# Optimization experiments

Measured on AMD Instinct MI355X. Metric: run time of the kernel, lower is better.

The kernel has to match this reference:

```python
import jax, jax.numpy as jnp
import numpy as np

HIDDEN = 512
HEADS = 8
PREFIX = 1  # prefix_size: rows >= PREFIX may not attend to cols < PREFIX (except causal tril already zeroed those only partially)


def setup_inputs() -> dict:
    key = jax.random.key(0)
    k1, k2, k3 = jax.random.split(key, 3)
    B, L, D = 2, 4096, HIDDEN
    x = jax.random.normal(k1, (B, L, D), dtype=jnp.float32)
    # torch Linear(hidden, 3*hidden): y = x @ W^T + b; we store W^T directly as [D, 3D]
    w_in = jax.random.normal(k2, (D, 3 * D), dtype=jnp.float32) * (1.0 / np.sqrt(D))
    b_in = jnp.zeros((3 * D,), dtype=jnp.float32)
    w_out = jax.random.normal(k3, (D, D), dtype=jnp.float32) * (1.0 / np.sqrt(D))
    b_out = jnp.zeros((D,), dtype=jnp.float32)
    return {"x": x, "w_in": w_in, "b_in": b_in, "w_out": w_out, "b_out": b_out}


def _prefix_causal_mask(L):
    # tril(ones) then zero out [prefix:, :prefix]
    m = jnp.tril(jnp.ones((L, L), dtype=bool))
    m = m.at[PREFIX:, :PREFIX].set(False)
    return m  # True = attend allowed


def reference(x, w_in, b_in, w_out, b_out):
    B, L, D = x.shape
    H, hd = HEADS, D // HEADS
    qkv = x @ w_in + b_in  # [B, L, 3D]
    q, k, v = jnp.split(qkv, 3, axis=-1)
    q = q.reshape(B, L, H, hd).transpose(0, 2, 1, 3)  # [B,H,L,hd]
    k = k.reshape(B, L, H, hd).transpose(0, 2, 1, 3)
    v = v.reshape(B, L, H, hd).transpose(0, 2, 1, 3)
    scale = 1.0 / np.sqrt(hd).astype(np.float32)
    attn = jnp.einsum('bhqd,bhkd->bhqk', q, k) * scale  # [B,H,L,L]
    mask = _prefix_causal_mask(L)
    attn = jnp.where(mask[None, None, :, :], attn, -jnp.inf)
    attn = jax.nn.softmax(attn, axis=-1)  # dropout p=0.0 -> identity
    out = jnp.einsum('bhqk,bhkd->bhqd', attn, v)  # [B,H,L,hd]
    out = out.transpose(0, 2, 1, 3).reshape(B, L, D)
    return out @ w_out + b_out
```

## Files before the change

kernel.cpp:

```cpp
#include <hip/hip_runtime.h>
#include <hip/hip_bf16.h>

#define BSZ   2
#define LSEQ  4096
#define DH    512
#define NH    8
#define HDIM  64

typedef unsigned short ushort_t;
typedef __attribute__((ext_vector_type(8))) short s8v;
typedef __attribute__((ext_vector_type(4))) short s4v;
typedef __attribute__((ext_vector_type(4))) float f4v;

#define C_EXP 0.18033688011112042f

__device__ __forceinline__ ushort_t f2bf(float f) {
    __hip_bfloat16 h = __float2bfloat16(f);
    return *(ushort_t*)&h;
}

__device__ __forceinline__ unsigned int fbits(float f) {
    union { float f; unsigned int u; } c; c.f = f; return c.u;
}

__device__ __forceinline__ unsigned int pk_trunc(float lo, float hi) {
    return (fbits(lo) >> 16) | (fbits(hi) & 0xFFFF0000u);
}

__device__ __forceinline__ void gld_lds16(const ushort_t* g, ushort_t* l) {
    __builtin_amdgcn_global_load_lds(
        (const __attribute__((address_space(1))) void*)g,
        (__attribute__((address_space(3))) void*)l, 16, 0, 0);
}

__device__ __forceinline__ void transpose_tile(const float* __restrict__ src,
                                               ushort_t* __restrict__ dst,
                                               int R, int C, int bx, int by)
{
    __shared__ float tile[32][33];
    int r0 = by * 32, c0 = bx * 32;
    int t = threadIdx.x;
    int tr = t >> 5, tc = t & 31;
    #pragma unroll
    for (int i = 0; i < 4; i++)
        tile[tr + 8 * i][tc] = src[(size_t)(r0 + tr + 8 * i) * C + c0 + tc];
    __syncthreads();
    #pragma unroll
    for (int i = 0; i < 4; i++) {
        int oc = tr + 8 * i;
        dst[(size_t)(c0 + oc) * R + r0 + tc] = f2bf(tile[tc][oc]);
    }
}

__global__ __launch_bounds__(256) void prep(const float* __restrict__ x,
                                            ushort_t* __restrict__ xb,
                                            const float* __restrict__ w_in,
                                            ushort_t* __restrict__ w_inT,
                                            const float* __restrict__ w_out,
                                            ushort_t* __restrict__ w_outT,
                                            float* __restrict__ Oacc,
                                            float* __restrict__ lacc)
{
    int bx = blockIdx.x;
    if (bx < 4096) {
        int i = (bx * 256 + threadIdx.x) * 4;
        float4 v = *(const float4*)&x[i];
        ushort_t o[4] = {f2bf(v.x), f2bf(v.y), f2bf(v.z), f2bf(v.w)};
        *(uint2*)&xb[i] = *(uint2*)o;
    } else if (bx < 4864) {
        int idx = bx - 4096;
        transpose_tile(w_in, w_inT, DH, 3 * DH, idx % 48, idx / 48);
    } else if (bx < 5120) {
        int idx = bx - 4864;
        transpose_tile(w_out, w_outT, DH, DH, idx % 16, idx / 16);
    } else if (bx < 9216) {
        int i = ((bx - 5120) * 256 + threadIdx.x) * 4;
        float4 z = {0.f, 0.f, 0.f, 0.f};
        *(float4*)&Oacc[i] = z;
    } else {
        int i = ((bx - 9216) * 256 + threadIdx.x) * 4;
        float4 z = {0.f, 0.f, 0.f, 0.f};
        *(float4*)&lacc[i] = z;
    }
}

template <typename OUT, bool QSCALE, bool VTRANS>
__global__ __launch_bounds__(256) void gemm_bt(const ushort_t* __restrict__ A,
                                               const ushort_t* __restrict__ Bt,
                                               const float* __restrict__ bias,
                                               OUT* __restrict__ C,
                                               ushort_t* __restrict__ vtout,
                                               int M, int N, int K)
{
    __shared__ ushort_t As[128 * 32];
    __shared__ ushort_t Bs[128 * 32];
    const int tid = threadIdx.x;
    const int row0 = blockIdx.y * 128, col0 = blockIdx.x * 128;
    const int wid = tid >> 6, lane = tid & 63;
    const int wm = wid >> 1, wn = wid & 1;
    const int quad = lane >> 4, ln = lane & 15;

    f4v acc[4][4] = {};

    const int srow = (lane >> 2);
    const int scol = (lane & 3) * 8;

    for (int k0 = 0; k0 < K; k0 += 32) {
        #pragma unroll
        for (int t = 0; t < 2; t++) {
            int chunk = wid * 2 + t;
            int r = chunk * 16 + srow;
            gld_lds16(&A[(size_t)(row0 + r) * K + k0 + scol], &As[chunk * 512]);
            gld_lds16(&Bt[(size_t)(col0 + r) * K + k0 + scol], &Bs[chunk * 512]);
        }
        __syncthreads();
        s8v af[4], bf[4];
        #pragma unroll
        for (int mt = 0; mt < 4; mt++)
            af[mt] = *(const s8v*)&As[(wm * 64 + mt * 16 + ln) * 32 + quad * 8];
        #pragma unroll
        for (int nt = 0; nt < 4; nt++)
            bf[nt] = *(const s8v*)&Bs[(wn * 64 + nt * 16 + ln) * 32 + quad * 8];
        #pragma unroll
        for (int mt = 0; mt < 4; mt++)
            #pragma unroll
            for (int nt = 0; nt < 4; nt++)
                acc[mt][nt] = __builtin_amdgcn_mfma_f32_16x16x32_bf16(
                    af[mt], bf[nt], acc[mt][nt], 0, 0, 0);
        __syncthreads();
    }

    #pragma unroll
    for (int mt = 0; mt < 4; mt++) {
        #pragma unroll
        for (int nt = 0; nt < 4; nt++) {
            int c = col0 + wn * 64 + nt * 16 + ln;
            float bv = bias[c];
            float scl = 1.0f;
            if constexpr (QSCALE) scl = (c < DH) ? C_EXP : 1.0f;
            bool vcol = false;
            if constexpr (VTRANS) vcol = (c >= 2 * DH);
            if (vcol) {
                int d = c - 2 * DH;
                int hh = d >> 6, dd = d & 63;
                int r0 = row0 + wm * 64 + mt * 16 + quad * 4;
                int bb = r0 >> 12, l = r0 & (LSEQ - 1);
                ushort_t tmp[4];
                #pragma unroll
                for (int reg = 0; reg < 4; reg++)
                    tmp[reg] = f2bf(acc[mt][nt][reg] + bv);
                *(uint2*)&vtout[((size_t)((bb * NH + hh) * 64 + dd)) * LSEQ + l]
                    = *(uint2*)tmp;
            } else {
                #pragma unroll
                for (int reg = 0; reg < 4; reg++) {
                    int r = row0 + wm * 64 + mt * 16 + quad * 4 + reg;
                    float v = (acc[mt][nt][reg] + bv) * scl;
                    if constexpr (sizeof(OUT) == 2)
                        C[(size_t)r * N + c] = (OUT)f2bf(v);
                    else
                        C[(size_t)r * N + c] = v;
                }
            }
        }
    }
}

__global__ __launch_bounds__(128) void flash_mfma(const ushort_t* __restrict__ qkv,
                                                  const ushort_t* __restrict__ vt,
                                                  float* __restrict__ Oacc,
                                                  float* __restrict__ lacc)
{
    __shared__ ushort_t Ks[64 * 72];
    __shared__ ushort_t Vs[64 * 72];

    const int p     = blockIdx.x >> 1;
    const int khalf = blockIdx.x & 1;
    const int h = blockIdx.y, b = blockIdx.z;
    const int tid = threadIdx.x;
    const int w = tid >> 6, lane = tid & 63;
    const int quad = lane >> 4, ln = lane & 15;

    const int sr = tid >> 1, sc = (tid & 1) * 32;
    const int ldsw = sr * 72 + sc;
    const size_t kstep = (size_t)64 * 3 * DH;

    const int qts[2] = {63 - p, p};

    for (int ti = 0; ti < 2; ti++) {
        const int qt = qts[ti], q0 = qt * 64;
        const int qrow0 = q0 + w * 32;
        const int n = qt + 1;
        const int ktBeg = khalf ? ((n + 1) >> 1) : 0;
        const int ktEnd = khalf ? n : ((n + 1) >> 1);

        s8v qa[2][2];
        #pragma unroll
        for (int qg = 0; qg < 2; qg++) {
            const ushort_t* qrow = qkv
                + ((size_t)(b * LSEQ + qrow0 + qg * 16 + ln)) * (3 * DH) + h * HDIM;
            qa[qg][0] = *(const s8v*)(qrow + quad * 8);
            qa[qg][1] = *(const s8v*)(qrow + 32 + quad * 8);
        }

        float l_s[2] = {0.0f, 0.0f};
        f4v o_acc[2][4] = {};

        if (ktBeg < ktEnd) {
            size_t gk = ((size_t)(b * LSEQ + ktBeg * 64 + sr)) * (3 * DH) + DH + h * HDIM + sc;
            size_t gv = ((size_t)((b * NH + h) * 64 + sr)) * LSEQ + ktBeg * 64 + sc;
            uint4 pk0 = *(const uint4*)&qkv[gk];
            uint4 pk1 = *(const uint4*)&qkv[gk + 8];
            uint4 pk2 = *(const uint4*)&qkv[gk + 16];
            uint4 pk3 = *(const uint4*)&qkv[gk + 24];
            uint4 pv0 = *(const uint4*)&vt[gv];
            uint4 pv1 = *(const uint4*)&vt[gv + 8];
            uint4 pv2 = *(const uint4*)&vt[gv + 16];
            uint4 pv3 = *(const uint4*)&vt[gv + 24];

            for (int kt = ktBeg; kt < ktEnd; kt++) {
                const int k0 = kt * 64;
                __syncthreads();
                *(uint4*)&Ks[ldsw]      = pk0;
                *(uint4*)&Ks[ldsw + 8]  = pk1;
                *(uint4*)&Ks[ldsw + 16] = pk2;
                *(uint4*)&Ks[ldsw + 24] = pk3;
                *(uint4*)&Vs[ldsw]      = pv0;
                *(uint4*)&Vs[ldsw + 8]  = pv1;
                *(uint4*)&Vs[ldsw + 16] = pv2;
                *(uint4*)&Vs[ldsw + 24] = pv3;
                if (kt + 1 < ktEnd) {
                    gk += kstep; gv += 64;
                    pk0 = *(const uint4*)&qkv[gk];
                    pk1 = *(const uint4*)&qkv[gk + 8];
                    pk2 = *(const uint4*)&qkv[gk + 16];
                    pk3 = *(const uint4*)&qkv[gk + 24];
                    pv0 = *(const uint4*)&vt[gv];
                    pv1 = *(const uint4*)&vt[gv + 8];
                    pv2 = *(const uint4*)&vt[gv + 16];
                    pv3 = *(const uint4*)&vt[gv + 24];
                }
                __syncthreads();

                s8v kb[4][2];
                #pragma unroll
                for (int nt = 0; nt < 4; nt++) {
                    kb[nt][0] = *(const s8v*)&Ks[(nt * 16 + ln) * 72 + quad * 8];
                    kb[nt][1] = *(const s8v*)&Ks[(nt * 16 + ln) * 72 + 32 + quad * 8];
                }
                s4v vf[4][4];
                #pragma unroll
                for (int dt = 0; dt < 4; dt++)
                    #pragma unroll
                    for (int nt = 0; nt < 4; nt++)
                        vf[dt][nt] = *(const s4v*)&Vs[(dt * 16 + ln) * 72 + nt * 16 + quad * 4];

                #pragma unroll
                for (int qg = 0; qg < 2; qg++) {
                    f4v s[4] = {};
                    #pragma unroll
                    for (int nt = 0; nt < 4; nt++) {
                        s[nt] = __builtin_amdgcn_mfma_f32_16x16x32_bf16(kb[nt][0], qa[qg][0], s[nt], 0, 0, 0);
                        s[nt] = __builtin_amdgcn_mfma_f32_16x16x32_bf16(kb[nt][1], qa[qg][1], s[nt], 0, 0, 0);
                    }

                    float pp[4][4];
                    const int q = qrow0 + qg * 16 + ln;
                    if (kt == qt) {
                        #pragma unroll
                        for (int nt = 0; nt < 4; nt++) {
                            #pragma unroll
                            for (int reg = 0; reg < 4; reg++) {
                                int kidx = k0 + nt * 16 + quad * 4 + reg;
                                bool valid = (kidx <= q) && (kidx >= 1 || q == 0);
                                pp[nt][reg] = valid ? __builtin_amdgcn_exp2f(s[nt][reg]) : 0.0f;
                            }
                        }
                    } else {
                        #pragma unroll
                        for (int nt = 0; nt < 4; nt++)
                            #pragma unroll
                            for (int reg = 0; reg < 4; reg++)
                                pp[nt][reg] = __builtin_amdgcn_exp2f(s[nt][reg]);
                        if (kt == 0 && quad == 0)
                            pp[0][0] = 0.0f;
                    }

                    #pragma unroll
                    for (int nt = 0; nt < 4; nt++)
                        l_s[qg] += (pp[nt][0] + pp[nt][1]) + (pp[nt][2] + pp[nt][3]);

                    #pragma unroll
                    for (int nt = 0; nt < 4; nt++) {
                        union { unsigned int u[2]; s4v v; } pk;
                        pk.u[0] = pk_trunc(pp[nt][0], pp[nt][1]);
                        pk.u[1] = pk_trunc(pp[nt][2], pp[nt][3]);
                        #pragma unroll
                        for (int dt = 0; dt < 4; dt++)
                            o_acc[qg][dt] = __builtin_amdgcn_mfma_f32_16x16x16bf16_1k(
                                pk.v, vf[dt][nt], o_acc[qg][dt], 0, 0, 0);
                    }
                }
            }
        }

        #pragma unroll
        for (int qg = 0; qg < 2; qg++) {
            float lf = l_s[qg];
            lf += __shfl_xor(lf, 16);
            lf += __shfl_xor(lf, 32);
            if (quad == 0)
                atomicAdd(&lacc[((size_t)(b * NH + h)) * LSEQ + qrow0 + qg * 16 + ln], lf);
            #pragma unroll
            for (int dt = 0; dt < 4; dt++)
                #pragma unroll
                for (int reg = 0; reg < 4; reg++)
                    atomicAdd(&Oacc[((size_t)(b * LSEQ + qrow0 + qg * 16 + quad * 4 + reg)) * DH
                                    + h * HDIM + dt * 16 + ln],
                              o_acc[qg][dt][reg]);
        }
    }
}

__global__ __launch_bounds__(256) void normalize(const float* __restrict__ Oacc,
                                                 const float* __restrict__ lacc,
                                                 ushort_t* __restrict__ att)
{
    int t = blockIdx.x * 256 + threadIdx.x;
    int row = t >> 5;
    int col0 = (t & 31) * 16;
    int h = col0 >> 6;
    int b = row >> 12, l = row & (LSEQ - 1);
    float linv = 1.0f / lacc[((size_t)(b * NH + h)) * LSEQ + l];
    const float* o = &Oacc[(size_t)row * DH + col0];
    ushort_t tmp[16];
    #pragma unroll
    for (int j = 0; j < 16; j++) tmp[j] = f2bf(o[j] * linv);
    size_t g = (size_t)row * DH + col0;
    *(uint4*)&att[g]     = *(uint4*)&tmp[0];
    *(uint4*)&att[g + 8] = *(uint4*)&tmp[8];
}

extern "C" void kernel_launch(void* const* d_in, const int* in_sizes, int n_in,
                              void* d_out, int out_size, void* d_ws, size_t ws_size,
                              hipStream_t stream)
{
    const float* x     = (const float*)d_in[0];
    const float* w_in  = (const float*)d_in[1];
    const float* b_in  = (const float*)d_in[2];
    const float* w_out = (const float*)d_in[3];
    const float* b_out = (const float*)d_in[4];
    float* out = (float*)d_out;

    const int M = BSZ * LSEQ;
    char* ws = (char*)d_ws;
    ushort_t* xb    = (ushort_t*)ws;                       ws += (size_t)M * DH * 2;
    ushort_t* w_inT = (ushort_t*)ws;                       ws += (size_t)3 * DH * DH * 2;
    ushort_t* w_outT= (ushort_t*)ws;                       ws += (size_t)DH * DH * 2;
    ushort_t* qkvb  = (ushort_t*)ws;                       ws += (size_t)M * 3 * DH * 2;
    ushort_t* vtb   = (ushort_t*)ws;                       ws += (size_t)M * DH * 2;
    ushort_t* attb  = (ushort_t*)ws;                       ws += (size_t)M * DH * 2;
    float*    Oacc  = (float*)ws;                          ws += (size_t)M * DH * 4;
    float*    lacc  = (float*)ws;

    prep<<<9280, 256, 0, stream>>>(x, xb, w_in, w_inT, w_out, w_outT, Oacc, lacc);

    gemm_bt<ushort_t, true, true><<<dim3(3 * DH / 128, M / 128), 256, 0, stream>>>(
        xb, w_inT, b_in, qkvb, vtb, M, 3 * DH, DH);

    flash_mfma<<<dim3(64, NH, BSZ), 128, 0, stream>>>(qkvb, vtb, Oacc, lacc);

    normalize<<<1024, 256, 0, stream>>>(Oacc, lacc, attb);

    gemm_bt<float, false, false><<<dim3(DH / 128, M / 128), 256, 0, stream>>>(
        attb, w_outT, b_out, out, nullptr, M, DH, DH);
}
```

Measured before the change: 186.1 us.

## Double-buffer K/V tiles in LDS and raise wave priority around MFMA

```diff
diff --git a/kernel.cpp b/kernel.cpp
--- a/kernel.cpp
+++ b/kernel.cpp
@@ -171,8 +171,8 @@
                                                   float* __restrict__ Oacc,
                                                   float* __restrict__ lacc)
 {
-    __shared__ ushort_t Ks[64 * 72];
-    __shared__ ushort_t Vs[64 * 72];
+    __shared__ ushort_t Ks[2][64 * 72];
+    __shared__ ushort_t Vs[2][64 * 72];
 
     const int p     = blockIdx.x >> 1;
     const int khalf = blockIdx.x & 1;
@@ -218,51 +218,78 @@
             uint4 pv2 = *(const uint4*)&vt[gv + 16];
             uint4 pv3 = *(const uint4*)&vt[gv + 24];
 
+            __syncthreads();
+            *(uint4*)&Ks[0][ldsw]      = pk0;
+            *(uint4*)&Ks[0][ldsw + 8]  = pk1;
+            *(uint4*)&Ks[0][ldsw + 16] = pk2;
+            *(uint4*)&Ks[0][ldsw + 24] = pk3;
+            *(uint4*)&Vs[0][ldsw]      = pv0;
+            *(uint4*)&Vs[0][ldsw + 8]  = pv1;
+            *(uint4*)&Vs[0][ldsw + 16] = pv2;
+            *(uint4*)&Vs[0][ldsw + 24] = pv3;
+            if (ktBeg + 1 < ktEnd) {
+                gk += kstep; gv += 64;
+                pk0 = *(const uint4*)&qkv[gk];
+                pk1 = *(const uint4*)&qkv[gk + 8];
+                pk2 = *(const uint4*)&qkv[gk + 16];
+                pk3 = *(const uint4*)&qkv[gk + 24];
+                pv0 = *(const uint4*)&vt[gv];
+                pv1 = *(const uint4*)&vt[gv + 8];
+                pv2 = *(const uint4*)&vt[gv + 16];
+                pv3 = *(const uint4*)&vt[gv + 24];
+            }
+
+            int cur = 0;
             for (int kt = ktBeg; kt < ktEnd; kt++) {
                 const int k0 = kt * 64;
                 __syncthreads();
-                *(uint4*)&Ks[ldsw]      = pk0;
-                *(uint4*)&Ks[ldsw + 8]  = pk1;
-                *(uint4*)&Ks[ldsw + 16] = pk2;
-                *(uint4*)&Ks[ldsw + 24] = pk3;
-                *(uint4*)&Vs[ldsw]      = pv0;
-                *(uint4*)&Vs[ldsw + 8]  = pv1;
-                *(uint4*)&Vs[ldsw + 16] = pv2;
-                *(uint4*)&Vs[ldsw + 24] = pv3;
-                if (kt + 1 < ktEnd) {
-                    gk += kstep; gv += 64;
-                    pk0 = *(const uint4*)&qkv[gk];
-                    pk1 = *(const uint4*)&qkv[gk + 8];
-                    pk2 = *(const uint4*)&qkv[gk + 16];
-                    pk3 = *(const uint4*)&qkv[gk + 24];
-                    pv0 = *(const uint4*)&vt[gv];
-                    pv1 = *(const uint4*)&vt[gv + 8];
-                    pv2 = *(const uint4*)&vt[gv + 16];
-                    pv3 = *(const uint4*)&vt[gv + 24];
-                }
-                __syncthreads();
 
                 s8v kb[4][2];
                 #pragma unroll
                 for (int nt = 0; nt < 4; nt++) {
-                    kb[nt][0] = *(const s8v*)&Ks[(nt * 16 + ln) * 72 + quad * 8];
-                    kb[nt][1] = *(const s8v*)&Ks[(nt * 16 + ln) * 72 + 32 + quad * 8];
+                    kb[nt][0] = *(const s8v*)&Ks[cur][(nt * 16 + ln) * 72 + quad * 8];
+                    kb[nt][1] = *(const s8v*)&Ks[cur][(nt * 16 + ln) * 72 + 32 + quad * 8];
                 }
                 s4v vf[4][4];
                 #pragma unroll
                 for (int dt = 0; dt < 4; dt++)
                     #pragma unroll
                     for (int nt = 0; nt < 4; nt++)
-                        vf[dt][nt] = *(const s4v*)&Vs[(dt * 16 + ln) * 72 + nt * 16 + quad * 4];
+                        vf[dt][nt] = *(const s4v*)&Vs[cur][(dt * 16 + ln) * 72 + nt * 16 + quad * 4];
+
+                if (kt + 1 < ktEnd) {
+                    const int nb = cur ^ 1;
+                    *(uint4*)&Ks[nb][ldsw]      = pk0;
+                    *(uint4*)&Ks[nb][ldsw + 8]  = pk1;
+                    *(uint4*)&Ks[nb][ldsw + 16] = pk2;
+                    *(uint4*)&Ks[nb][ldsw + 24] = pk3;
+                    *(uint4*)&Vs[nb][ldsw]      = pv0;
+                    *(uint4*)&Vs[nb][ldsw + 8]  = pv1;
+                    *(uint4*)&Vs[nb][ldsw + 16] = pv2;
+                    *(uint4*)&Vs[nb][ldsw + 24] = pv3;
+                    if (kt + 2 < ktEnd) {
+                        gk += kstep; gv += 64;
+                        pk0 = *(const uint4*)&qkv[gk];
+                        pk1 = *(const uint4*)&qkv[gk + 8];
+                        pk2 = *(const uint4*)&qkv[gk + 16];
+                        pk3 = *(const uint4*)&qkv[gk + 24];
+                        pv0 = *(const uint4*)&vt[gv];
+                        pv1 = *(const uint4*)&vt[gv + 8];
+                        pv2 = *(const uint4*)&vt[gv + 16];
+                        pv3 = *(const uint4*)&vt[gv + 24];
+                    }
+                }
 
                 #pragma unroll
                 for (int qg = 0; qg < 2; qg++) {
                     f4v s[4] = {};
+                    __builtin_amdgcn_s_setprio(1);
                     #pragma unroll
                     for (int nt = 0; nt < 4; nt++) {
                         s[nt] = __builtin_amdgcn_mfma_f32_16x16x32_bf16(kb[nt][0], qa[qg][0], s[nt], 0, 0, 0);
                         s[nt] = __builtin_amdgcn_mfma_f32_16x16x32_bf16(kb[nt][1], qa[qg][1], s[nt], 0, 0, 0);
                     }
+                    __builtin_amdgcn_s_setprio(0);
 
                     float pp[4][4];
                     const int q = qrow0 + qg * 16 + ln;
@@ -290,6 +317,7 @@
                     for (int nt = 0; nt < 4; nt++)
                         l_s[qg] += (pp[nt][0] + pp[nt][1]) + (pp[nt][2] + pp[nt][3]);
 
+                    __builtin_amdgcn_s_setprio(1);
                     #pragma unroll
                     for (int nt = 0; nt < 4; nt++) {
                         union { unsigned int u[2]; s4v v; } pk;
@@ -300,7 +328,9 @@
                             o_acc[qg][dt] = __builtin_amdgcn_mfma_f32_16x16x16bf16_1k(
                                 pk.v, vf[dt][nt], o_acc[qg][dt], 0, 0, 0);
                     }
+                    __builtin_amdgcn_s_setprio(0);
                 }
+                cur ^= 1;
             }
         }
 
```

New measurement: 191.9 us. 1.03x slower.

## Split flash attention query tile across four waves and add MFMA priority hints

Applied to the files above, without the earlier changes.

```diff
diff --git a/kernel.cpp b/kernel.cpp
--- a/kernel.cpp
+++ b/kernel.cpp
@@ -166,7 +166,7 @@
     }
 }
 
-__global__ __launch_bounds__(128) void flash_mfma(const ushort_t* __restrict__ qkv,
+__global__ __launch_bounds__(256) void flash_mfma(const ushort_t* __restrict__ qkv,
                                                   const ushort_t* __restrict__ vt,
                                                   float* __restrict__ Oacc,
                                                   float* __restrict__ lacc)
@@ -181,7 +181,7 @@
     const int w = tid >> 6, lane = tid & 63;
     const int quad = lane >> 4, ln = lane & 15;
 
-    const int sr = tid >> 1, sc = (tid & 1) * 32;
+    const int sr = tid >> 2, sc = (tid & 3) * 16;
     const int ldsw = sr * 72 + sc;
     const size_t kstep = (size_t)64 * 3 * DH;
 
@@ -189,56 +189,43 @@
 
     for (int ti = 0; ti < 2; ti++) {
         const int qt = qts[ti], q0 = qt * 64;
-        const int qrow0 = q0 + w * 32;
+        const int qrow0 = q0 + w * 16;
         const int n = qt + 1;
         const int ktBeg = khalf ? ((n + 1) >> 1) : 0;
         const int ktEnd = khalf ? n : ((n + 1) >> 1);
 
-        s8v qa[2][2];
-        #pragma unroll
-        for (int qg = 0; qg < 2; qg++) {
+        s8v qa[2];
+        {
             const ushort_t* qrow = qkv
-                + ((size_t)(b * LSEQ + qrow0 + qg * 16 + ln)) * (3 * DH) + h * HDIM;
-            qa[qg][0] = *(const s8v*)(qrow + quad * 8);
-            qa[qg][1] = *(const s8v*)(qrow + 32 + quad * 8);
-        }
-
-        float l_s[2] = {0.0f, 0.0f};
-        f4v o_acc[2][4] = {};
+                + ((size_t)(b * LSEQ + qrow0 + ln)) * (3 * DH) + h * HDIM;
+            qa[0] = *(const s8v*)(qrow + quad * 8);
+            qa[1] = *(const s8v*)(qrow + 32 + quad * 8);
+        }
+
+        float l_s = 0.0f;
+        f4v o_acc[4] = {};
 
         if (ktBeg < ktEnd) {
             size_t gk = ((size_t)(b * LSEQ + ktBeg * 64 + sr)) * (3 * DH) + DH + h * HDIM + sc;
             size_t gv = ((size_t)((b * NH + h) * 64 + sr)) * LSEQ + ktBeg * 64 + sc;
             uint4 pk0 = *(const uint4*)&qkv[gk];
             uint4 pk1 = *(const uint4*)&qkv[gk + 8];
-            uint4 pk2 = *(const uint4*)&qkv[gk + 16];
-            uint4 pk3 = *(const uint4*)&qkv[gk + 24];
             uint4 pv0 = *(const uint4*)&vt[gv];
             uint4 pv1 = *(const uint4*)&vt[gv + 8];
-            uint4 pv2 = *(const uint4*)&vt[gv + 16];
-            uint4 pv3 = *(const uint4*)&vt[gv + 24];
 
             for (int kt = ktBeg; kt < ktEnd; kt++) {
                 const int k0 = kt * 64;
                 __syncthreads();
                 *(uint4*)&Ks[ldsw]      = pk0;
                 *(uint4*)&Ks[ldsw + 8]  = pk1;
-                *(uint4*)&Ks[ldsw + 16] = pk2;
-                *(uint4*)&Ks[ldsw + 24] = pk3;
                 *(uint4*)&Vs[ldsw]      = pv0;
                 *(uint4*)&Vs[ldsw + 8]  = pv1;
-                *(uint4*)&Vs[ldsw + 16] = pv2;
-                *(uint4*)&Vs[ldsw + 24] = pv3;
                 if (kt + 1 < ktEnd) {
                     gk += kstep; gv += 64;
                     pk0 = *(const uint4*)&qkv[gk];
                     pk1 = *(const uint4*)&qkv[gk + 8];
-                    pk2 = *(const uint4*)&qkv[gk + 16];
-                    pk3 = *(const uint4*)&qkv[gk + 24];
                     pv0 = *(const uint4*)&vt[gv];
                     pv1 = *(const uint4*)&vt[gv + 8];
-                    pv2 = *(const uint4*)&vt[gv + 16];
-                    pv3 = *(const uint4*)&vt[gv + 24];
                 }
                 __syncthreads();
 
@@ -255,69 +242,69 @@
                     for (int nt = 0; nt < 4; nt++)
                         vf[dt][nt] = *(const s4v*)&Vs[(dt * 16 + ln) * 72 + nt * 16 + quad * 4];
 
-                #pragma unroll
-                for (int qg = 0; qg < 2; qg++) {
-                    f4v s[4] = {};
+                f4v s[4] = {};
+                __builtin_amdgcn_s_setprio(1);
+                #pragma unroll
+                for (int nt = 0; nt < 4; nt++) {
+                    s[nt] = __builtin_amdgcn_mfma_f32_16x16x32_bf16(kb[nt][0], qa[0], s[nt], 0, 0, 0);
+                    s[nt] = __builtin_amdgcn_mfma_f32_16x16x32_bf16(kb[nt][1], qa[1], s[nt], 0, 0, 0);
+                }
+                __builtin_amdgcn_s_setprio(0);
+
+                float pp[4][4];
+                const int q = qrow0 + ln;
+                if (kt == qt) {
                     #pragma unroll
                     for (int nt = 0; nt < 4; nt++) {
-                        s[nt] = __builtin_amdgcn_mfma_f32_16x16x32_bf16(kb[nt][0], qa[qg][0], s[nt], 0, 0, 0);
-                        s[nt] = __builtin_amdgcn_mfma_f32_16x16x32_bf16(kb[nt][1], qa[qg][1], s[nt], 0, 0, 0);
+                        #pragma unroll
+                        for (int reg = 0; reg < 4; reg++) {
+                            int kidx = k0 + nt * 16 + quad * 4 + reg;
+                            bool valid = (kidx <= q) && (kidx >= 1 || q == 0);
+                            pp[nt][reg] = valid ? __builtin_amdgcn_exp2f(s[nt][reg]) : 0.0f;
+                        }
                     }
-
-                    float pp[4][4];
-                    const int q = qrow0 + qg * 16 + ln;
-                    if (kt == qt) {
-                        #pragma unroll
-                        for (int nt = 0; nt < 4; nt++) {
-                            #pragma unroll
-                            for (int reg = 0; reg < 4; reg++) {
-                                int kidx = k0 + nt * 16 + quad * 4 + reg;
-                                bool valid = (kidx <= q) && (kidx >= 1 || q == 0);
-                                pp[nt][reg] = valid ? __builtin_amdgcn_exp2f(s[nt][reg]) : 0.0f;
-                            }
-                        }
-                    } else {
-                        #pragma unroll
-                        for (int nt = 0; nt < 4; nt++)
-                            #pragma unroll
-                            for (int reg = 0; reg < 4; reg++)
-                                pp[nt][reg] = __builtin_amdgcn_exp2f(s[nt][reg]);
-                        if (kt == 0 && quad == 0)
-                            pp[0][0] = 0.0f;
-                    }
-
+                } else {
                     #pragma unroll
                     for (int nt = 0; nt < 4; nt++)
-                        l_s[qg] += (pp[nt][0] + pp[nt][1]) + (pp[nt][2] + pp[nt][3]);
-
+                        #pragma unroll
+                        for (int reg = 0; reg < 4; reg++)
+                            pp[nt][reg] = __builtin_amdgcn_exp2f(s[nt][reg]);
+                    if (kt == 0 && quad == 0)
+                        pp[0][0] = 0.0f;
+                }
+
+                #pragma unroll
+                for (int nt = 0; nt < 4; nt++)
+                    l_s += (pp[nt][0] + pp[nt][1]) + (pp[nt][2] + pp[nt][3]);
+
+                __builtin_amdgcn_s_setprio(1);
+                #pragma unroll
+                for (int nt = 0; nt < 4; nt++) {
+                    union { unsigned int u[2]; s4v v; } pk;
+                    pk.u[0] = pk_trunc(pp[nt][0], pp[nt][1]);
+                    pk.u[1] = pk_trunc(pp[nt][2], pp[nt][3]);
                     #pragma unroll
-                    for (int nt = 0; nt < 4; nt++) {
-                        union { unsigned int u[2]; s4v v; } pk;
-                        pk.u[0] = pk_trunc(pp[nt][0], pp[nt][1]);
-                        pk.u[1] = pk_trunc(pp[nt][2], pp[nt][3]);
-                        #pragma unroll
-                        for (int dt = 0; dt < 4; dt++)
-                            o_acc[qg][dt] = __builtin_amdgcn_mfma_f32_16x16x16bf16_1k(
-                                pk.v, vf[dt][nt], o_acc[qg][dt], 0, 0, 0);
-                    }
-                }
+                    for (int dt = 0; dt < 4; dt++)
+                        o_acc[dt] = __builtin_amdgcn_mfma_f32_16x16x16bf16_1k(
+                            pk.v, vf[dt][nt], o_acc[dt], 0, 0, 0);
+                }
+                __builtin_amdgcn_s_setprio(0);
             }
         }
 
-        #pragma unroll
-        for (int qg = 0; qg < 2; qg++) {
-            float lf = l_s[qg];
+        {
+            float lf = l_s;
             lf += __shfl_xor(lf, 16);
             lf += __shfl_xor(lf, 32);
             if (quad == 0)
-                atomicAdd(&lacc[((size_t)(b * NH + h)) * LSEQ + qrow0 + qg * 16 + ln], lf);
+                atomicAdd(&lacc[((size_t)(b * NH + h)) * LSEQ + qrow0 + ln], lf);
             #pragma unroll
             for (int dt = 0; dt < 4; dt++)
                 #pragma unroll
                 for (int reg = 0; reg < 4; reg++)
-                    atomicAdd(&Oacc[((size_t)(b * LSEQ + qrow0 + qg * 16 + quad * 4 + reg)) * DH
+                    atomicAdd(&Oacc[((size_t)(b * LSEQ + qrow0 + quad * 4 + reg)) * DH
                                     + h * HDIM + dt * 16 + ln],
-                              o_acc[qg][dt][reg]);
+                              o_acc[dt][reg]);
         }
     }
 }
@@ -368,7 +355,7 @@
     gemm_bt<ushort_t, true, true><<<dim3(3 * DH / 128, M / 128), 256, 0, stream>>>(
         xb, w_inT, b_in, qkvb, vtb, M, 3 * DH, DH);
 
-    flash_mfma<<<dim3(64, NH, BSZ), 128, 0, stream>>>(qkvb, vtb, Oacc, lacc);
+    flash_mfma<<<dim3(64, NH, BSZ), 256, 0, stream>>>(qkvb, vtb, Oacc, lacc);
 
     normalize<<<1024, 256, 0, stream>>>(Oacc, lacc, attb);
 
```

Result: slower. 199.2 us (+7.1%).

## Share K/V tiles across paired query tiles with interleaved key split

Applied to the files above, without the earlier changes.

```diff
diff --git a/kernel.cpp b/kernel.cpp
--- a/kernel.cpp
+++ b/kernel.cpp
@@ -174,9 +174,13 @@
     __shared__ ushort_t Ks[64 * 72];
     __shared__ ushort_t Vs[64 * 72];
 
-    const int p     = blockIdx.x >> 1;
-    const int khalf = blockIdx.x & 1;
+    const int x = blockIdx.x;
     const int h = blockIdx.y, b = blockIdx.z;
+    const int parity = x & 1;
+    const int p = ((x >> 1) + h * 4 + (b << 4)) & 31;
+    const int qtA = 63 - p, qtB = p;
+    const int nA = qtA + 1, nB = qtB + 1;
+
     const int tid = threadIdx.x;
     const int w = tid >> 6, lane = tid & 63;
     const int quad = lane >> 4, ln = lane & 15;
@@ -185,139 +189,145 @@
     const int ldsw = sr * 72 + sc;
     const size_t kstep = (size_t)64 * 3 * DH;
 
-    const int qts[2] = {63 - p, p};
-
-    for (int ti = 0; ti < 2; ti++) {
-        const int qt = qts[ti], q0 = qt * 64;
-        const int qrow0 = q0 + w * 32;
-        const int n = qt + 1;
-        const int ktBeg = khalf ? ((n + 1) >> 1) : 0;
-        const int ktEnd = khalf ? n : ((n + 1) >> 1);
-
-        s8v qa[2][2];
+    const int qrow0A = qtA * 64 + w * 32;
+    const int qrow0B = qtB * 64 + w * 32;
+
+    s8v qa[2][2][2];
+    #pragma unroll
+    for (int t = 0; t < 2; t++) {
+        const int qr0 = t ? qrow0B : qrow0A;
         #pragma unroll
         for (int qg = 0; qg < 2; qg++) {
             const ushort_t* qrow = qkv
-                + ((size_t)(b * LSEQ + qrow0 + qg * 16 + ln)) * (3 * DH) + h * HDIM;
-            qa[qg][0] = *(const s8v*)(qrow + quad * 8);
-            qa[qg][1] = *(const s8v*)(qrow + 32 + quad * 8);
-        }
-
-        float l_s[2] = {0.0f, 0.0f};
-        f4v o_acc[2][4] = {};
-
-        if (ktBeg < ktEnd) {
-            size_t gk = ((size_t)(b * LSEQ + ktBeg * 64 + sr)) * (3 * DH) + DH + h * HDIM + sc;
-            size_t gv = ((size_t)((b * NH + h) * 64 + sr)) * LSEQ + ktBeg * 64 + sc;
-            uint4 pk0 = *(const uint4*)&qkv[gk];
-            uint4 pk1 = *(const uint4*)&qkv[gk + 8];
-            uint4 pk2 = *(const uint4*)&qkv[gk + 16];
-            uint4 pk3 = *(const uint4*)&qkv[gk + 24];
-            uint4 pv0 = *(const uint4*)&vt[gv];
-            uint4 pv1 = *(const uint4*)&vt[gv + 8];
-            uint4 pv2 = *(const uint4*)&vt[gv + 16];
-            uint4 pv3 = *(const uint4*)&vt[gv + 24];
-
-            for (int kt = ktBeg; kt < ktEnd; kt++) {
-                const int k0 = kt * 64;
-                __syncthreads();
-                *(uint4*)&Ks[ldsw]      = pk0;
-                *(uint4*)&Ks[ldsw + 8]  = pk1;
-                *(uint4*)&Ks[ldsw + 16] = pk2;
-                *(uint4*)&Ks[ldsw + 24] = pk3;
-                *(uint4*)&Vs[ldsw]      = pv0;
-                *(uint4*)&Vs[ldsw + 8]  = pv1;
-                *(uint4*)&Vs[ldsw + 16] = pv2;
-                *(uint4*)&Vs[ldsw + 24] = pv3;
-                if (kt + 1 < ktEnd) {
-                    gk += kstep; gv += 64;
-                    pk0 = *(const uint4*)&qkv[gk];
-                    pk1 = *(const uint4*)&qkv[gk + 8];
-                    pk2 = *(const uint4*)&qkv[gk + 16];
-                    pk3 = *(const uint4*)&qkv[gk + 24];
-                    pv0 = *(const uint4*)&vt[gv];
-                    pv1 = *(const uint4*)&vt[gv + 8];
-                    pv2 = *(const uint4*)&vt[gv + 16];
-                    pv3 = *(const uint4*)&vt[gv + 24];
+                + ((size_t)(b * LSEQ + qr0 + qg * 16 + ln)) * (3 * DH) + h * HDIM;
+            qa[t][qg][0] = *(const s8v*)(qrow + quad * 8);
+            qa[t][qg][1] = *(const s8v*)(qrow + 32 + quad * 8);
+        }
+    }
+
+    float l_s[2][2] = {};
+    f4v o_acc[2][2][4] = {};
+
+    size_t gk = ((size_t)(b * LSEQ + parity * 64 + sr)) * (3 * DH) + DH + h * HDIM + sc;
+    size_t gv = ((size_t)((b * NH + h) * 64 + sr)) * LSEQ + parity * 64 + sc;
+    uint4 pk0 = *(const uint4*)&qkv[gk];
+    uint4 pk1 = *(const uint4*)&qkv[gk + 8];
+    uint4 pk2 = *(const uint4*)&qkv[gk + 16];
+    uint4 pk3 = *(const uint4*)&qkv[gk + 24];
+    uint4 pv0 = *(const uint4*)&vt[gv];
+    uint4 pv1 = *(const uint4*)&vt[gv + 8];
+    uint4 pv2 = *(const uint4*)&vt[gv + 16];
+    uint4 pv3 = *(const uint4*)&vt[gv + 24];
+
+    for (int kt = parity; kt < nA; kt += 2) {
+        const int k0 = kt * 64;
+        __syncthreads();
+        *(uint4*)&Ks[ldsw]      = pk0;
+        *(uint4*)&Ks[ldsw + 8]  = pk1;
+        *(uint4*)&Ks[ldsw + 16] = pk2;
+        *(uint4*)&Ks[ldsw + 24] = pk3;
+        *(uint4*)&Vs[ldsw]      = pv0;
+        *(uint4*)&Vs[ldsw + 8]  = pv1;
+        *(uint4*)&Vs[ldsw + 16] = pv2;
+        *(uint4*)&Vs[ldsw + 24] = pv3;
+        if (kt + 2 < nA) {
+            gk += 2 * kstep; gv += 128;
+            pk0 = *(const uint4*)&qkv[gk];
+            pk1 = *(const uint4*)&qkv[gk + 8];
+            pk2 = *(const uint4*)&qkv[gk + 16];
+            pk3 = *(const uint4*)&qkv[gk + 24];
+            pv0 = *(const uint4*)&vt[gv];
+            pv1 = *(const uint4*)&vt[gv + 8];
+            pv2 = *(const uint4*)&vt[gv + 16];
+            pv3 = *(const uint4*)&vt[gv + 24];
+        }
+        __syncthreads();
+
+        s8v kb[4][2];
+        #pragma unroll
+        for (int nt = 0; nt < 4; nt++) {
+            kb[nt][0] = *(const s8v*)&Ks[(nt * 16 + ln) * 72 + quad * 8];
+            kb[nt][1] = *(const s8v*)&Ks[(nt * 16 + ln) * 72 + 32 + quad * 8];
+        }
+        s4v vf[4][4];
+        #pragma unroll
+        for (int dt = 0; dt < 4; dt++)
+            #pragma unroll
+            for (int nt = 0; nt < 4; nt++)
+                vf[dt][nt] = *(const s4v*)&Vs[(dt * 16 + ln) * 72 + nt * 16 + quad * 4];
+
+        auto do_tile = [&](int qt_, int qrow0_, s8v (&qa_)[2][2],
+                           float (&ls_)[2], f4v (&oa_)[2][4]) {
+            #pragma unroll
+            for (int qg = 0; qg < 2; qg++) {
+                f4v s[4] = {};
+                #pragma unroll
+                for (int nt = 0; nt < 4; nt++) {
+                    s[nt] = __builtin_amdgcn_mfma_f32_16x16x32_bf16(kb[nt][0], qa_[qg][0], s[nt], 0, 0, 0);
+                    s[nt] = __builtin_amdgcn_mfma_f32_16x16x32_bf16(kb[nt][1], qa_[qg][1], s[nt], 0, 0, 0);
                 }
-                __syncthreads();
-
-                s8v kb[4][2];
-                #pragma unroll
-                for (int nt = 0; nt < 4; nt++) {
-                    kb[nt][0] = *(const s8v*)&Ks[(nt * 16 + ln) * 72 + quad * 8];
-                    kb[nt][1] = *(const s8v*)&Ks[(nt * 16 + ln) * 72 + 32 + quad * 8];
-                }
-                s4v vf[4][4];
-                #pragma unroll
-                for (int dt = 0; dt < 4; dt++)
+
+                float pp[4][4];
+                const int q = qrow0_ + qg * 16 + ln;
+                if (kt == qt_) {
+                    #pragma unroll
+                    for (int nt = 0; nt < 4; nt++) {
+                        #pragma unroll
+                        for (int reg = 0; reg < 4; reg++) {
+                            int kidx = k0 + nt * 16 + quad * 4 + reg;
+                            bool valid = (kidx <= q) && (kidx >= 1 || q == 0);
+                            pp[nt][reg] = valid ? __builtin_amdgcn_exp2f(s[nt][reg]) : 0.0f;
+                        }
+                    }
+                } else {
                     #pragma unroll
                     for (int nt = 0; nt < 4; nt++)
-                        vf[dt][nt] = *(const s4v*)&Vs[(dt * 16 + ln) * 72 + nt * 16 + quad * 4];
-
-                #pragma unroll
-                for (int qg = 0; qg < 2; qg++) {
-                    f4v s[4] = {};
+                        #pragma unroll
+                        for (int reg = 0; reg < 4; reg++)
+                            pp[nt][reg] = __builtin_amdgcn_exp2f(s[nt][reg]);
+                    if (kt == 0 && quad == 0)
+                        pp[0][0] = 0.0f;
+                }
+
+                #pragma unroll
+                for (int nt = 0; nt < 4; nt++)
+                    ls_[qg] += (pp[nt][0] + pp[nt][1]) + (pp[nt][2] + pp[nt][3]);
+
+                #pragma unroll
+                for (int nt = 0; nt < 4; nt++) {
+                    union { unsigned int u[2]; s4v v; } pk;
+                    pk.u[0] = pk_trunc(pp[nt][0], pp[nt][1]);
+                    pk.u[1] = pk_trunc(pp[nt][2], pp[nt][3]);
                     #pragma unroll
-                    for (int nt = 0; nt < 4; nt++) {
-                        s[nt] = __builtin_amdgcn_mfma_f32_16x16x32_bf16(kb[nt][0], qa[qg][0], s[nt], 0, 0, 0);
-                        s[nt] = __builtin_amdgcn_mfma_f32_16x16x32_bf16(kb[nt][1], qa[qg][1], s[nt], 0, 0, 0);
-                    }
-
-                    float pp[4][4];
-                    const int q = qrow0 + qg * 16 + ln;
-                    if (kt == qt) {
-                        #pragma unroll
-                        for (int nt = 0; nt < 4; nt++) {
-                            #pragma unroll
-                            for (int reg = 0; reg < 4; reg++) {
-                                int kidx = k0 + nt * 16 + quad * 4 + reg;
-                                bool valid = (kidx <= q) && (kidx >= 1 || q == 0);
-                                pp[nt][reg] = valid ? __builtin_amdgcn_exp2f(s[nt][reg]) : 0.0f;
-                            }
-                        }
-                    } else {
-                        #pragma unroll
-                        for (int nt = 0; nt < 4; nt++)
-                            #pragma unroll
-                            for (int reg = 0; reg < 4; reg++)
-                                pp[nt][reg] = __builtin_amdgcn_exp2f(s[nt][reg]);
-                        if (kt == 0 && quad == 0)
-                            pp[0][0] = 0.0f;
-                    }
-
-                    #pragma unroll
-                    for (int nt = 0; nt < 4; nt++)
-                        l_s[qg] += (pp[nt][0] + pp[nt][1]) + (pp[nt][2] + pp[nt][3]);
-
-                    #pragma unroll
-                    for (int nt = 0; nt < 4; nt++) {
-                        union { unsigned int u[2]; s4v v; } pk;
-                        pk.u[0] = pk_trunc(pp[nt][0], pp[nt][1]);
-                        pk.u[1] = pk_trunc(pp[nt][2], pp[nt][3]);
-                        #pragma unroll
-                        for (int dt = 0; dt < 4; dt++)
-                            o_acc[qg][dt] = __builtin_amdgcn_mfma_f32_16x16x16bf16_1k(
-                                pk.v, vf[dt][nt], o_acc[qg][dt], 0, 0, 0);
-                    }
+                    for (int dt = 0; dt < 4; dt++)
+                        oa_[qg][dt] = __builtin_amdgcn_mfma_f32_16x16x16bf16_1k(
+                            pk.v, vf[dt][nt], oa_[qg][dt], 0, 0, 0);
                 }
             }
-        }
-
+        };
+
+        do_tile(qtA, qrow0A, qa[0], l_s[0], o_acc[0]);
+        if (kt < nB)
+            do_tile(qtB, qrow0B, qa[1], l_s[1], o_acc[1]);
+    }
+
+    #pragma unroll
+    for (int t = 0; t < 2; t++) {
+        const int qr0 = t ? qrow0B : qrow0A;
         #pragma unroll
         for (int qg = 0; qg < 2; qg++) {
-            float lf = l_s[qg];
+            float lf = l_s[t][qg];
             lf += __shfl_xor(lf, 16);
             lf += __shfl_xor(lf, 32);
             if (quad == 0)
-                atomicAdd(&lacc[((size_t)(b * NH + h)) * LSEQ + qrow0 + qg * 16 + ln], lf);
+                atomicAdd(&lacc[((size_t)(b * NH + h)) * LSEQ + qr0 + qg * 16 + ln], lf);
             #pragma unroll
             for (int dt = 0; dt < 4; dt++)
                 #pragma unroll
                 for (int reg = 0; reg < 4; reg++)
-                    atomicAdd(&Oacc[((size_t)(b * LSEQ + qrow0 + qg * 16 + quad * 4 + reg)) * DH
+                    atomicAdd(&Oacc[((size_t)(b * LSEQ + qr0 + qg * 16 + quad * 4 + reg)) * DH
                                     + h * HDIM + dt * 16 + ln],
-                              o_acc[qg][dt][reg]);
+                              o_acc[t][qg][dt][reg]);
         }
     }
 }
```

New measurement: 202.9 us. 1.09x slower.
